# Optimization experiments

Measured on AMD Instinct MI355X. Metric: run time of the kernel, lower is better.

## Reference

```python
import jax, jax.numpy as jnp
import numpy as np

NUM_HEADS = 8


def setup_inputs() -> dict:
    key = jax.random.key(0)
    ks = jax.random.split(key, 9)
    B, S, E = 16, 2048, 768
    s = 0.02
    return {
        "features": jax.random.normal(ks[0], (B, S, E), jnp.float32),
        "in_proj_w": jax.random.normal(ks[1], (3 * E, E), jnp.float32) * s,
        "in_proj_b": jnp.zeros((3 * E,), jnp.float32),
        "out_proj_w": jax.random.normal(ks[2], (E, E), jnp.float32) * s,
        "out_proj_b": jnp.zeros((E,), jnp.float32),
        "w1": jax.random.normal(ks[3], (384, E), jnp.float32) * s,
        "b1": jnp.zeros((384,), jnp.float32),
        "w2": jax.random.normal(ks[4], (1, 384), jnp.float32) * s,
        "b2": jnp.zeros((1,), jnp.float32),
    }


def reference(features, in_proj_w, in_proj_b, out_proj_w, out_proj_b, w1, b1, w2, b2):
    # torch nn.MultiheadAttention default batch_first=False: dim 0 is the
    # attended sequence axis (length B here), dim 1 is the MHA batch (S).
    B, S, E = features.shape
    H = NUM_HEADS
    Dh = E // H
    qkv = features @ in_proj_w.T + in_proj_b          # (B, S, 3E)
    q, k, v = jnp.split(qkv, 3, axis=-1)
    q = q.reshape(B, S, H, Dh)
    k = k.reshape(B, S, H, Dh)
    v = v.reshape(B, S, H, Dh)
    scale = 1.0 / jnp.sqrt(jnp.asarray(Dh, features.dtype))
    # attention over axis-0 positions (l, m in 0..B-1), per (s, h)
    scores = jnp.einsum('lshd,mshd->shlm', q * scale, k)
    attn = jax.nn.softmax(scores, axis=-1)
    ctx = jnp.einsum('shlm,mshd->lshd', attn, v).reshape(B, S, E)
    attn_out = ctx @ out_proj_w.T + out_proj_b        # (B, S, E)
    # batched 2-layer MLP (replaces the Python per-row loop)
    h = jax.nn.relu(attn_out @ w1.T + b1)             # (B, S, 384)
    prob = h @ w2.T + b2                              # (B, S, 1)
    contacts = jnp.broadcast_to(prob, (B, S, S))      # contacts[:, i, :] = prob[:, i]
    return contacts
```

## Files before the change

kernel.cpp:

```cpp
#include <hip/hip_runtime.h>

typedef unsigned short u16;
typedef __attribute__((ext_vector_type(8))) __bf16 bf16x8;
typedef __attribute__((ext_vector_type(4))) float floatx4;

#define B_DIM  16
#define S_DIM  2048
#define E_DIM  768
#define HEADS  8
#define DHEAD  96
#define MROWS  32768
#define QKV_LD 2304
#define ATT_ST 392

__device__ __forceinline__ u16 f2b(float f) {
    unsigned u = __float_as_uint(f);
    u += 0x7fffu + ((u >> 16) & 1u);
    return (u16)(u >> 16);
}
__device__ __forceinline__ float blo(unsigned u) { return __uint_as_float(u << 16); }
__device__ __forceinline__ float bhi(unsigned u) { return __uint_as_float(u & 0xffff0000u); }

__device__ __forceinline__ void axpy8(float* acc, float p, uint4 v) {
    acc[0] += p * blo(v.x); acc[1] += p * bhi(v.x);
    acc[2] += p * blo(v.y); acc[3] += p * bhi(v.y);
    acc[4] += p * blo(v.z); acc[5] += p * bhi(v.z);
    acc[6] += p * blo(v.w); acc[7] += p * bhi(v.w);
}

#define PB0 24576
#define PB1 26304
#define PB2 26592
#define PB3 27168
#define PB4 27552
__global__ __launch_bounds__(256) void prep(const float* __restrict__ features,
                                            const float* __restrict__ in_proj_w,
                                            const float* __restrict__ w1,
                                            const float* __restrict__ out_proj_w,
                                            const float* __restrict__ bo,
                                            const float* __restrict__ b1,
                                            u16* __restrict__ fbf, u16* __restrict__ wib,
                                            u16* __restrict__ w1b, u16* __restrict__ WoT,
                                            float* __restrict__ cbuf) {
    __shared__ float tsh[32][33];
    const int b = blockIdx.x, tid = threadIdx.x;
    if (b < PB2) {
        const float* src; u16* dst; long i;
        if (b < PB0)      { src = features;  dst = fbf; i = (long)b * 256 + tid; }
        else if (b < PB1) { src = in_proj_w; dst = wib; i = (long)(b - PB0) * 256 + tid; }
        else              { src = w1;        dst = w1b; i = (long)(b - PB1) * 256 + tid; }
        float4 f = ((const float4*)src)[i];
        ushort4 r;
        r.x = f2b(f.x); r.y = f2b(f.y); r.z = f2b(f.z); r.w = f2b(f.w);
        ((ushort4*)dst)[i] = r;
    } else if (b < PB3) {
        const int t = b - PB2;
        const int bxT = t % 24, byT = t / 24;
        const int tx = tid & 31, ty = tid >> 5;
        int x = bxT * 32 + tx;
        int y = byT * 32 + ty;
#pragma unroll
        for (int j = 0; j < 4; j++) tsh[ty + j * 8][tx] = out_proj_w[(long)(y + j * 8) * 768 + x];
        __syncthreads();
        x = byT * 32 + tx;
        y = bxT * 32 + ty;
#pragma unroll
        for (int j = 0; j < 4; j++) WoT[(long)(y + j * 8) * 768 + x] = f2b(tsh[tx][ty + j * 8]);
    } else {
        const int n = b - PB3;
        const float* row = w1 + (long)n * 768;
        float s = row[tid] * bo[tid] + row[tid + 256] * bo[tid + 256] + row[tid + 512] * bo[tid + 512];
#pragma unroll
        for (int off = 32; off > 0; off >>= 1) s += __shfl_xor(s, off);
        if ((tid & 63) == 0) tsh[0][tid >> 6] = s;
        __syncthreads();
        if (tid == 0) cbuf[n] = tsh[0][0] + tsh[0][1] + tsh[0][2] + tsh[0][3] + b1[n];
    }
}

template<bool PERM, bool SWIZ>
__global__ __launch_bounds__(256) void gemm_bt(const u16* __restrict__ A, int lda,
                                               const u16* __restrict__ W,
                                               const float* __restrict__ bias,
                                               u16* __restrict__ Cout, int ldc,
                                               int N, int K) {
    __shared__ __align__(16) u16 sA[128 * 32];
    __shared__ __align__(16) u16 sB[128 * 32];
    __shared__ __align__(16) u16 sC[32 * 132];
    const int tid  = threadIdx.x;
    int bn, bm;
    if (SWIZ) {
        const int bx  = blockIdx.x;
        const int xcd = bx & 7;
        const int q   = bx >> 3;
        const int s   = q / 144;
        const int r   = q % 144;
        bn = r >> 3;
        bm = s * 64 + xcd * 8 + (r & 7);
    } else {
        bn = blockIdx.x;
        bm = blockIdx.y;
    }
    const int lane = tid & 63;
    const int wid  = tid >> 6;
    const int wm   = (wid >> 1) * 64;
    const int wn   = (wid & 1) * 64;
    const int ar = tid >> 2;
    const int ac = (tid & 3) * 8;
    const u16* Ap = A + (long)(bm * 128 + ar) * lda + ac;
    const u16* Wp = W + (long)(bn * 128 + ar) * K + ac;
    const long a2 = (long)64 * lda;
    const long w2 = (long)64 * K;

    floatx4 acc[4][4] = {};
    const int fr = lane & 15;
    const int fq = (lane >> 4) * 8;

    for (int k0 = 0; k0 < K; k0 += 32) {
        __builtin_amdgcn_global_load_lds((const __attribute__((address_space(1))) void*)(Ap + k0),
                                         (__attribute__((address_space(3))) void*)(sA + tid * 8), 16, 0, 0);
        __builtin_amdgcn_global_load_lds((const __attribute__((address_space(1))) void*)(Ap + a2 + k0),
                                         (__attribute__((address_space(3))) void*)(sA + 2048 + tid * 8), 16, 0, 0);
        __builtin_amdgcn_global_load_lds((const __attribute__((address_space(1))) void*)(Wp + k0),
                                         (__attribute__((address_space(3))) void*)(sB + tid * 8), 16, 0, 0);
        __builtin_amdgcn_global_load_lds((const __attribute__((address_space(1))) void*)(Wp + w2 + k0),
                                         (__attribute__((address_space(3))) void*)(sB + 2048 + tid * 8), 16, 0, 0);
        __syncthreads();

        bf16x8 aF[4], bF[4];
#pragma unroll
        for (int i = 0; i < 4; i++) {
            aF[i] = *(const bf16x8*)(sA + (wm + i * 16 + fr) * 32 + fq);
            bF[i] = *(const bf16x8*)(sB + (wn + i * 16 + fr) * 32 + fq);
        }
#pragma unroll
        for (int i = 0; i < 4; i++)
#pragma unroll
            for (int j = 0; j < 4; j++)
                acc[i][j] = __builtin_amdgcn_mfma_f32_16x16x32_bf16(aF[i], bF[j], acc[i][j], 0, 0, 0);
        __syncthreads();
    }

    const int rq = (lane >> 4) * 4;
    float bvj[4];
#pragma unroll
    for (int j = 0; j < 4; j++)
        bvj[j] = bias ? bias[bn * 128 + wn + j * 16 + fr] : 0.f;
#pragma unroll
    for (int p = 0; p < 4; p++) {
        if ((p >> 1) == (wid >> 1)) {
#pragma unroll
            for (int ii = 0; ii < 2; ii++) {
                const int i = (p & 1) * 2 + ii;
#pragma unroll
                for (int j = 0; j < 4; j++) {
                    const int col = wn + j * 16 + fr;
#pragma unroll
                    for (int r = 0; r < 4; r++)
                        sC[(ii * 16 + rq + r) * 132 + col] = f2b(acc[i][j][r] + bvj[j]);
                }
            }
        }
        __syncthreads();
#pragma unroll
        for (int q2 = 0; q2 < 2; q2++) {
            const int lr = (tid >> 4) + q2 * 16;
            const int c  = tid & 15;
            uint4 v = *(const uint4*)(sC + lr * 132 + c * 8);
            const int rl = bm * 128 + p * 32 + lr;
            const long grow = PERM ? (long)(((rl & 2047) << 4) | (rl >> 11)) : (long)rl;
            *(uint4*)(Cout + grow * ldc + bn * 128 + c * 8) = v;
        }
        __syncthreads();
    }
}

__global__ __launch_bounds__(256) void attn_kernel(u16* __restrict__ qkv) {
    __shared__ __align__(16) u16 sQ[16 * ATT_ST], sK[16 * ATT_ST], sV[16 * ATT_ST];
    __shared__ float sS[4][16][16];
    const int tid = threadIdx.x;
    const int s  = blockIdx.x >> 1;
    const int hh = blockIdx.x & 1;
    const u16* base = qkv + (long)s * 16 * QKV_LD + hh * 384;

#pragma unroll
    for (int it = 0; it < 9; it++) {
        const int i = it * 256 + tid;
        const int t = i / 768, rem = i % 768, l = rem / 48, c = rem % 48;
        const u16* src = base + (long)l * QKV_LD + t * E_DIM + c * 8;
        u16* dst = (t == 0 ? sQ : t == 1 ? sK : sV) + l * ATT_ST + c * 8;
        *(uint4*)dst = *(const uint4*)src;
    }
    __syncthreads();

    const int lane = tid & 63;
    const int w    = tid >> 6;
    const int fr   = lane & 15;
    const int fq   = (lane >> 4) * 8;
    floatx4 acc = {};
    const u16* qrow = sQ + fr * ATT_ST + w * DHEAD + fq;
    const u16* krow = sK + fr * ATT_ST + w * DHEAD + fq;
#pragma unroll
    for (int st = 0; st < 3; st++) {
        bf16x8 qa = *(const bf16x8*)(qrow + st * 32);
        bf16x8 kb = *(const bf16x8*)(krow + st * 32);
        acc = __builtin_amdgcn_mfma_f32_16x16x32_bf16(qa, kb, acc, 0, 0, 0);
    }
    const int rq = (lane >> 4) * 4;
#pragma unroll
    for (int r = 0; r < 4; r++) {
        float sc = acc[r] * 0.10206207261596577f;
        float mx = sc;
#pragma unroll
        for (int off = 8; off > 0; off >>= 1) mx = fmaxf(mx, __shfl_xor(mx, off));
        float e = __expf(sc - mx);
        float sum = e;
#pragma unroll
        for (int off = 8; off > 0; off >>= 1) sum += __shfl_xor(sum, off);
        sS[w][rq + r][fr] = e / sum;
    }
    __syncthreads();

#pragma unroll
    for (int j = 0; j < 3; j++) {
        const int task = j * 256 + tid;
        const int h = task / 192, rem = task % 192, ll = rem / 12, c = rem % 12;
        float a[8] = {};
#pragma unroll
        for (int mm = 0; mm < 16; mm++) {
            const float p = sS[h][ll][mm];
            uint4 vw = *(const uint4*)(sV + mm * ATT_ST + h * DHEAD + c * 8);
            axpy8(a, p, vw);
        }
        ushort4 o0, o1;
        o0.x = f2b(a[0]); o0.y = f2b(a[1]); o0.z = f2b(a[2]); o0.w = f2b(a[3]);
        o1.x = f2b(a[4]); o1.y = f2b(a[5]); o1.z = f2b(a[6]); o1.w = f2b(a[7]);
        u16* dst = qkv + ((long)s * 16 + ll) * QKV_LD + (hh * 4 + h) * DHEAD + c * 8;
        *(ushort4*)dst = o0;
        *(ushort4*)(dst + 4) = o1;
    }
}

__global__ __launch_bounds__(256) void mlp_gemm(const u16* __restrict__ A, int lda,
                                                const u16* __restrict__ G,
                                                const float* __restrict__ cbias,
                                                const float* __restrict__ w2,
                                                float* __restrict__ part) {
    __shared__ __align__(16) u16 sA[128 * 32];
    __shared__ __align__(16) u16 sB[128 * 32];
    __shared__ float rowsum[128];
    const int tid = threadIdx.x;
    const int bm  = blockIdx.x / 3;
    const int bn  = blockIdx.x % 3;
    if (tid < 128) rowsum[tid] = 0.f;
    const int lane = tid & 63;
    const int wid  = tid >> 6;
    const int wm   = (wid >> 1) * 64;
    const int wn   = (wid & 1) * 64;
    const int ar = tid >> 2;
    const int ac = (tid & 3) * 8;
    const u16* Ap = A + (long)(bm * 128 + ar) * lda + ac;
    const u16* Wp = G + (long)(bn * 128 + ar) * 768 + ac;
    const long a2 = (long)64 * lda;
    const int fr = lane & 15;
    const int fq = (lane >> 4) * 8;
    const int rq = (lane >> 4) * 4;

    floatx4 acc[4][4] = {};
    for (int k0 = 0; k0 < 768; k0 += 32) {
        __builtin_amdgcn_global_load_lds((const __attribute__((address_space(1))) void*)(Ap + k0),
                                         (__attribute__((address_space(3))) void*)(sA + tid * 8), 16, 0, 0);
        __builtin_amdgcn_global_load_lds((const __attribute__((address_space(1))) void*)(Ap + a2 + k0),
                                         (__attribute__((address_space(3))) void*)(sA + 2048 + tid * 8), 16, 0, 0);
        __builtin_amdgcn_global_load_lds((const __attribute__((address_space(1))) void*)(Wp + k0),
                                         (__attribute__((address_space(3))) void*)(sB + tid * 8), 16, 0, 0);
        __builtin_amdgcn_global_load_lds((const __attribute__((address_space(1))) void*)(Wp + (long)64 * 768 + k0),
                                         (__attribute__((address_space(3))) void*)(sB + 2048 + tid * 8), 16, 0, 0);
        __syncthreads();
        bf16x8 aF[4], bF[4];
#pragma unroll
        for (int i = 0; i < 4; i++) {
            aF[i] = *(const bf16x8*)(sA + (wm + i * 16 + fr) * 32 + fq);
            bF[i] = *(const bf16x8*)(sB + (wn + i * 16 + fr) * 32 + fq);
        }
#pragma unroll
        for (int i = 0; i < 4; i++)
#pragma unroll
            for (int j = 0; j < 4; j++)
                acc[i][j] = __builtin_amdgcn_mfma_f32_16x16x32_bf16(aF[i], bF[j], acc[i][j], 0, 0, 0);
        __syncthreads();
    }
    float partl[4][4] = {};
#pragma unroll
    for (int j = 0; j < 4; j++) {
        const int col = bn * 128 + wn + j * 16 + fr;
        const float cv = cbias[col];
        const float wv = w2[col];
#pragma unroll
        for (int i = 0; i < 4; i++)
#pragma unroll
            for (int r = 0; r < 4; r++)
                partl[i][r] += fmaxf(acc[i][j][r] + cv, 0.f) * wv;
    }
#pragma unroll
    for (int i = 0; i < 4; i++)
#pragma unroll
        for (int r = 0; r < 4; r++) {
            float v = partl[i][r];
#pragma unroll
            for (int off = 8; off > 0; off >>= 1) v += __shfl_xor(v, off);
            if (fr == 0) atomicAdd(&rowsum[wm + i * 16 + rq + r], v);
        }
    __syncthreads();
    if (tid < 128) part[(long)bn * MROWS + bm * 128 + tid] = rowsum[tid];
}

__global__ __launch_bounds__(256) void bcast_kernel(const float* __restrict__ part,
                                                    const float* __restrict__ b2,
                                                    float* __restrict__ out) {
    const int tid = threadIdx.x;
    const long p0 = (long)blockIdx.x * 4;
    const float b2v = b2[0];
#pragma unroll
    for (int r = 0; r < 4; r++) {
        const long p = p0 + r;
        const float pv = part[p] + part[MROWS + p] + part[2 * MROWS + p] + b2v;
        float4* dst = (float4*)(out + ((p & 15) * S_DIM + (p >> 4)) * S_DIM);
        float4 v4 = make_float4(pv, pv, pv, pv);
        dst[tid] = v4;
        dst[tid + 256] = v4;
    }
}

extern "C" void kernel_launch(void* const* d_in, const int* in_sizes, int n_in,
                              void* d_out, int out_size, void* d_ws, size_t ws_size,
                              hipStream_t stream) {
    const float* features   = (const float*)d_in[0];
    const float* in_proj_b  = (const float*)d_in[2];
    const float* out_proj_b = (const float*)d_in[4];
    const float* b1 = (const float*)d_in[6];
    const float* w2 = (const float*)d_in[7];
    const float* b2 = (const float*)d_in[8];
    float* out = (float*)d_out;

    char* p = (char*)d_ws;
    u16* fbf = (u16*)p; p += (size_t)MROWS * E_DIM * 2;
    u16* wib = (u16*)p; p += (size_t)QKV_LD * E_DIM * 2;
    u16* w1b = (u16*)p; p += (size_t)384 * E_DIM * 2;
    u16* WoT = (u16*)p; p += (size_t)E_DIM * E_DIM * 2;
    u16* Gbf = (u16*)p; p += (size_t)384 * E_DIM * 2;
    float* cbuf  = (float*)p; p += 384 * 4;
    float* partb = (float*)p; p += (size_t)3 * MROWS * 4;
    p = (char*)(((size_t)p + 255) & ~(size_t)255);
    u16* qkv = (u16*)p; p += (size_t)MROWS * QKV_LD * 2;
    u16* ctx = qkv;

    prep<<<PB4, 256, 0, stream>>>(features, (const float*)d_in[1], (const float*)d_in[5],
                                  (const float*)d_in[3], out_proj_b, b1,
                                  fbf, wib, w1b, WoT, cbuf);
    gemm_bt<false, false><<<dim3(6, 3), 256, 0, stream>>>(
        w1b, E_DIM, WoT, nullptr, Gbf, E_DIM, E_DIM, E_DIM);
    gemm_bt<true, true><<<dim3(4608), 256, 0, stream>>>(
        fbf, E_DIM, wib, in_proj_b, qkv, QKV_LD, QKV_LD, E_DIM);
    attn_kernel<<<S_DIM * 2, 256, 0, stream>>>(qkv);
    mlp_gemm<<<768, 256, 0, stream>>>(ctx, QKV_LD, Gbf, cbuf, w2, partb);
    bcast_kernel<<<MROWS / 4, 256, 0, stream>>>(partb, b2, out);
}
```

Baseline: 606.1 us.

## Double the K step per barrier in GEMMs and use nontemporal broadcast stores

Both bf16 GEMM kernels now load two 32-wide K slices into doubled LDS buffers per iteration. This halves the number of barrier pairs and gives more MFMA work between syncs. The broadcast kernel now uses one block per sequence position that writes all 16 batch rows with nontemporal stores, meant to cut cache pollution from the large output write. The larger LDS footprint may reduce occupancy in the GEMM kernels.

```diff
diff --git a/kernel.cpp b/kernel.cpp
--- a/kernel.cpp
+++ b/kernel.cpp
@@ -12,6 +12,10 @@
 #define MROWS  32768
 #define QKV_LD 2304
 #define ATT_ST 392
+
+#define GLDS(gp, lp) __builtin_amdgcn_global_load_lds( \
+    (const __attribute__((address_space(1))) void*)(gp), \
+    (__attribute__((address_space(3))) void*)(lp), 16, 0, 0)
 
 __device__ __forceinline__ u16 f2b(float f) {
     unsigned u = __float_as_uint(f);
@@ -84,8 +88,8 @@
                                                const float* __restrict__ bias,
                                                u16* __restrict__ Cout, int ldc,
                                                int N, int K) {
-    __shared__ __align__(16) u16 sA[128 * 32];
-    __shared__ __align__(16) u16 sB[128 * 32];
+    __shared__ __align__(16) u16 sA[2 * 128 * 32];
+    __shared__ __align__(16) u16 sB[2 * 128 * 32];
     __shared__ __align__(16) u16 sC[32 * 132];
     const int tid  = threadIdx.x;
     int bn, bm;
@@ -116,28 +120,29 @@
     const int fr = lane & 15;
     const int fq = (lane >> 4) * 8;
 
-    for (int k0 = 0; k0 < K; k0 += 32) {
-        __builtin_amdgcn_global_load_lds((const __attribute__((address_space(1))) void*)(Ap + k0),
-                                         (__attribute__((address_space(3))) void*)(sA + tid * 8), 16, 0, 0);
-        __builtin_amdgcn_global_load_lds((const __attribute__((address_space(1))) void*)(Ap + a2 + k0),
-                                         (__attribute__((address_space(3))) void*)(sA + 2048 + tid * 8), 16, 0, 0);
-        __builtin_amdgcn_global_load_lds((const __attribute__((address_space(1))) void*)(Wp + k0),
-                                         (__attribute__((address_space(3))) void*)(sB + tid * 8), 16, 0, 0);
-        __builtin_amdgcn_global_load_lds((const __attribute__((address_space(1))) void*)(Wp + w2 + k0),
-                                         (__attribute__((address_space(3))) void*)(sB + 2048 + tid * 8), 16, 0, 0);
-        __syncthreads();
-
-        bf16x8 aF[4], bF[4];
-#pragma unroll
-        for (int i = 0; i < 4; i++) {
-            aF[i] = *(const bf16x8*)(sA + (wm + i * 16 + fr) * 32 + fq);
-            bF[i] = *(const bf16x8*)(sB + (wn + i * 16 + fr) * 32 + fq);
-        }
-#pragma unroll
-        for (int i = 0; i < 4; i++)
-#pragma unroll
-            for (int j = 0; j < 4; j++)
-                acc[i][j] = __builtin_amdgcn_mfma_f32_16x16x32_bf16(aF[i], bF[j], acc[i][j], 0, 0, 0);
+    for (int k0 = 0; k0 < K; k0 += 64) {
+#pragma unroll
+        for (int h = 0; h < 2; h++) {
+            GLDS(Ap + k0 + h * 32,      sA + h * 4096 + tid * 8);
+            GLDS(Ap + a2 + k0 + h * 32, sA + h * 4096 + 2048 + tid * 8);
+            GLDS(Wp + k0 + h * 32,      sB + h * 4096 + tid * 8);
+            GLDS(Wp + w2 + k0 + h * 32, sB + h * 4096 + 2048 + tid * 8);
+        }
+        __syncthreads();
+#pragma unroll
+        for (int h = 0; h < 2; h++) {
+            bf16x8 aF[4], bF[4];
+#pragma unroll
+            for (int i = 0; i < 4; i++) {
+                aF[i] = *(const bf16x8*)(sA + h * 4096 + (wm + i * 16 + fr) * 32 + fq);
+                bF[i] = *(const bf16x8*)(sB + h * 4096 + (wn + i * 16 + fr) * 32 + fq);
+            }
+#pragma unroll
+            for (int i = 0; i < 4; i++)
+#pragma unroll
+                for (int j = 0; j < 4; j++)
+                    acc[i][j] = __builtin_amdgcn_mfma_f32_16x16x32_bf16(aF[i], bF[j], acc[i][j], 0, 0, 0);
+        }
         __syncthreads();
     }
 
@@ -246,8 +251,8 @@
                                                 const float* __restrict__ cbias,
                                                 const float* __restrict__ w2,
                                                 float* __restrict__ part) {
-    __shared__ __align__(16) u16 sA[128 * 32];
-    __shared__ __align__(16) u16 sB[128 * 32];
+    __shared__ __align__(16) u16 sA[2 * 128 * 32];
+    __shared__ __align__(16) u16 sB[2 * 128 * 32];
     __shared__ float rowsum[128];
     const int tid = threadIdx.x;
     const int bm  = blockIdx.x / 3;
@@ -262,32 +267,35 @@
     const u16* Ap = A + (long)(bm * 128 + ar) * lda + ac;
     const u16* Wp = G + (long)(bn * 128 + ar) * 768 + ac;
     const long a2 = (long)64 * lda;
+    const long w2s = (long)64 * 768;
     const int fr = lane & 15;
     const int fq = (lane >> 4) * 8;
     const int rq = (lane >> 4) * 4;
 
     floatx4 acc[4][4] = {};
-    for (int k0 = 0; k0 < 768; k0 += 32) {
-        __builtin_amdgcn_global_load_lds((const __attribute__((address_space(1))) void*)(Ap + k0),
-                                         (__attribute__((address_space(3))) void*)(sA + tid * 8), 16, 0, 0);
-        __builtin_amdgcn_global_load_lds((const __attribute__((address_space(1))) void*)(Ap + a2 + k0),
-                                         (__attribute__((address_space(3))) void*)(sA + 2048 + tid * 8), 16, 0, 0);
-        __builtin_amdgcn_global_load_lds((const __attribute__((address_space(1))) void*)(Wp + k0),
-                                         (__attribute__((address_space(3))) void*)(sB + tid * 8), 16, 0, 0);
-        __builtin_amdgcn_global_load_lds((const __attribute__((address_space(1))) void*)(Wp + (long)64 * 768 + k0),
-                                         (__attribute__((address_space(3))) void*)(sB + 2048 + tid * 8), 16, 0, 0);
-        __syncthreads();
-        bf16x8 aF[4], bF[4];
-#pragma unroll
-        for (int i = 0; i < 4; i++) {
-            aF[i] = *(const bf16x8*)(sA + (wm + i * 16 + fr) * 32 + fq);
-            bF[i] = *(const bf16x8*)(sB + (wn + i * 16 + fr) * 32 + fq);
-        }
-#pragma unroll
-        for (int i = 0; i < 4; i++)
-#pragma unroll
-            for (int j = 0; j < 4; j++)
-                acc[i][j] = __builtin_amdgcn_mfma_f32_16x16x32_bf16(aF[i], bF[j], acc[i][j], 0, 0, 0);
+    for (int k0 = 0; k0 < 768; k0 += 64) {
+#pragma unroll
+        for (int h = 0; h < 2; h++) {
+            GLDS(Ap + k0 + h * 32,       sA + h * 4096 + tid * 8);
+            GLDS(Ap + a2 + k0 + h * 32,  sA + h * 4096 + 2048 + tid * 8);
+            GLDS(Wp + k0 + h * 32,       sB + h * 4096 + tid * 8);
+            GLDS(Wp + w2s + k0 + h * 32, sB + h * 4096 + 2048 + tid * 8);
+        }
+        __syncthreads();
+#pragma unroll
+        for (int h = 0; h < 2; h++) {
+            bf16x8 aF[4], bF[4];
+#pragma unroll
+            for (int i = 0; i < 4; i++) {
+                aF[i] = *(const bf16x8*)(sA + h * 4096 + (wm + i * 16 + fr) * 32 + fq);
+                bF[i] = *(const bf16x8*)(sB + h * 4096 + (wn + i * 16 + fr) * 32 + fq);
+            }
+#pragma unroll
+            for (int i = 0; i < 4; i++)
+#pragma unroll
+                for (int j = 0; j < 4; j++)
+                    acc[i][j] = __builtin_amdgcn_mfma_f32_16x16x32_bf16(aF[i], bF[j], acc[i][j], 0, 0, 0);
+        }
         __syncthreads();
     }
     float partl[4][4] = {};
@@ -319,16 +327,16 @@
                                                     const float* __restrict__ b2,
                                                     float* __restrict__ out) {
     const int tid = threadIdx.x;
-    const long p0 = (long)blockIdx.x * 4;
+    const long s  = blockIdx.x;
     const float b2v = b2[0];
 #pragma unroll
-    for (int r = 0; r < 4; r++) {
-        const long p = p0 + r;
+    for (int l = 0; l < 16; l++) {
+        const long p = s * 16 + l;
         const float pv = part[p] + part[MROWS + p] + part[2 * MROWS + p] + b2v;
-        float4* dst = (float4*)(out + ((p & 15) * S_DIM + (p >> 4)) * S_DIM);
-        float4 v4 = make_float4(pv, pv, pv, pv);
-        dst[tid] = v4;
-        dst[tid + 256] = v4;
+        floatx4 v4 = {pv, pv, pv, pv};
+        floatx4* dst = (floatx4*)(out + ((long)l * S_DIM + s) * S_DIM);
+        __builtin_nontemporal_store(v4, dst + tid);
+        __builtin_nontemporal_store(v4, dst + tid + 256);
     }
 }
 
@@ -364,5 +372,5 @@
         fbf, E_DIM, wib, in_proj_b, qkv, QKV_LD, QKV_LD, E_DIM);
     attn_kernel<<<S_DIM * 2, 256, 0, stream>>>(qkv);
     mlp_gemm<<<768, 256, 0, stream>>>(ctx, QKV_LD, Gbf, cbuf, w2, partb);
-    bcast_kernel<<<MROWS / 4, 256, 0, stream>>>(partb, b2, out);
-}
+    bcast_kernel<<<S_DIM, 256, 0, stream>>>(partb, b2, out);
+}
```

Measured after the change: 591.5 us. 1.02x faster.
